# Optimization experiments

Measured on AMD Instinct MI355X. Metric: run time of the kernel, lower is better.

Reference implementation:

```python
import jax, jax.numpy as jnp
import numpy as np

N = 50000   # nodes
E = 800000  # edges (avg degree 16)
F_IN, F_HID, F_OUT = 4, 64, 1


def setup_inputs() -> dict:
    key = jax.random.key(0)
    k1, k2, k3, k4 = jax.random.split(key, 4)
    x = jax.random.normal(k1, (N, F_IN), dtype=jnp.float32)
    edge_index = jax.random.randint(k2, (2, E), 0, N, dtype=jnp.int64)
    W1 = jax.random.normal(k3, (F_IN, F_HID), dtype=jnp.float32) * (1.0 / np.sqrt(F_IN))
    b1 = jnp.zeros((F_HID,), dtype=jnp.float32)
    W2 = jax.random.normal(k4, (F_HID, F_OUT), dtype=jnp.float32) * (1.0 / np.sqrt(F_HID))
    b2 = jnp.zeros((F_OUT,), dtype=jnp.float32)
    return {"x": x, "edge_index": edge_index, "W1": W1, "b1": b1, "W2": W2, "b2": b2}


def _gcn_conv(h, W, b, src, dst, norm, n_nodes):
    # h: [N, F_in] -> linear -> gather src -> scale by norm -> scatter-add at dst
    m = (h @ W)[src] * norm[:, None]          # [E+N, F_out]
    out = jax.ops.segment_sum(m, dst, num_segments=n_nodes)
    return out + b


def reference(x, edge_index, W1, b1, W2, b2):
    n = x.shape[0]
    loops = jnp.arange(n, dtype=edge_index.dtype)
    src = jnp.concatenate([edge_index[0], loops])  # add self loops (PyG default)
    dst = jnp.concatenate([edge_index[1], loops])
    # symmetric normalization: deg computed at target (col) as in PyG gcn_norm
    deg = jax.ops.segment_sum(jnp.ones_like(dst, dtype=x.dtype), dst, num_segments=n)
    dis = jnp.where(deg > 0, deg ** -0.5, 0.0)
    norm = dis[src] * dis[dst]                      # [E+N]

    h = jax.nn.relu(_gcn_conv(x, W1, b1, src, dst, norm, n))
    # F.dropout with training=False (inference) is identity
    out = _gcn_conv(h, W2, b2, src, dst, norm, n)
    return jax.nn.sigmoid(out)                      # [N, 1]
```

## Files before the change

kernel.cpp:

```cpp
#include <hip/hip_runtime.h>


#define FH 64
#define NPC 256
#define NBC_MAX 256
#define CHB 8192
#define EPT 32
#define BCAP 8192
#define NPF 64

__global__ void k_fill(const int* __restrict__ src, const int* __restrict__ dst,
                       int* __restrict__ bcnt, unsigned int* __restrict__ ebuf,
                       int E, int nbc) {
    __shared__ int h[NBC_MAX];
    __shared__ int resv[NBC_MAX];
    int t = threadIdx.x;
    if (t < nbc) h[t] = 0;
    __syncthreads();
    int base = blockIdx.x * CHB;
    unsigned int pe[EPT];
    #pragma unroll
    for (int k = 0; k < EPT; ++k) {
        int e = base + k * 256 + t;
        if (e < E) {
            int d = dst[e];
            pe[k] = ((unsigned)d << 16) | (unsigned)src[e];
            atomicAdd(&h[d >> 8], 1);
        } else {
            pe[k] = 0xffffffffu;
        }
    }
    __syncthreads();
    if (t < nbc) {
        int c = h[t];
        resv[t] = c ? atomicAdd(&bcnt[t], c) : 0;
        h[t] = 0;
    }
    __syncthreads();
    #pragma unroll
    for (int k = 0; k < EPT; ++k) {
        if (pe[k] != 0xffffffffu) {
            int b = pe[k] >> 24;
            int idx = resv[b] + atomicAdd(&h[b], 1);
            if (idx < BCAP) ebuf[(size_t)b * BCAP + idx] = pe[k];
        }
    }
}

__global__ void k_finish1(const unsigned int* __restrict__ ebuf,
                          const int* __restrict__ bcnt,
                          const float* __restrict__ x, float* __restrict__ dis,
                          float* __restrict__ xd, int N) {
    __shared__ int lc[NPF];
    int f = blockIdx.x, t = threadIdx.x;
    int cb = f >> 2, w = f & 3;
    if (t < NPF) lc[t] = 0;
    __syncthreads();
    int c = min(bcnt[cb], BCAP);
    const unsigned int* eb = ebuf + (size_t)cb * BCAP;
    for (int j = t; j < c; j += 256) {
        int local = (eb[j] >> 16) & 255;
        if ((local >> 6) == w) atomicAdd(&lc[local & 63], 1);
    }
    __syncthreads();
    int node = f * NPF + t;
    if (t < NPF && node < N) {
        float dn = rsqrtf((float)(lc[t] + 1));
        dis[node] = dn;
        float4 xv = *reinterpret_cast<const float4*>(x + (size_t)node * 4);
        float4 o;
        o.x = dn * xv.x; o.y = dn * xv.y; o.z = dn * xv.z; o.w = dn * xv.w;
        *reinterpret_cast<float4*>(xd + (size_t)node * 4) = o;
    }
}

__global__ void k_agg(const unsigned int* __restrict__ ebuf,
                      const int* __restrict__ bcnt,
                      const float* __restrict__ xd, const float* __restrict__ dis,
                      const float* __restrict__ W1, const float* __restrict__ b1,
                      const float* __restrict__ W2, float* __restrict__ q, int N) {
    __shared__ float y4[NPF * 5];
    __shared__ float sW[4 * FH];
    __shared__ float sb1[FH];
    __shared__ float sW2[FH];
    int f = blockIdx.x, t = threadIdx.x;
    int cb = f >> 2, w = f & 3;
    sW[t] = W1[t];
    if (t < FH) { sb1[t] = b1[t]; sW2[t] = W2[t]; }
    if (t < NPF * 5) y4[t] = 0.0f;
    if (t + 256 < NPF * 5) y4[t + 256] = 0.0f;
    __syncthreads();
    int c = min(bcnt[cb], BCAP);
    const unsigned int* eb = ebuf + (size_t)cb * BCAP;
    for (int j = t; j < c; j += 256) {
        unsigned int pe = eb[j];
        int local = (pe >> 16) & 255;
        if ((local >> 6) == w) {
            int s = pe & 0xffff;
            float4 xv = *reinterpret_cast<const float4*>(xd + (size_t)s * 4);
            int l = local & 63;
            atomicAdd(&y4[l * 5 + 0], xv.x);
            atomicAdd(&y4[l * 5 + 1], xv.y);
            atomicAdd(&y4[l * 5 + 2], xv.z);
            atomicAdd(&y4[l * 5 + 3], xv.w);
        }
    }
    __syncthreads();
    int node = f * NPF + t;
    if (t < NPF && node < N) {
        float dn = dis[node];
        float4 xv = *reinterpret_cast<const float4*>(xd + (size_t)node * 4);
        float u0 = dn * (y4[t * 5 + 0] + xv.x);
        float u1 = dn * (y4[t * 5 + 1] + xv.y);
        float u2 = dn * (y4[t * 5 + 2] + xv.z);
        float u3 = dn * (y4[t * 5 + 3] + xv.w);
        float acc = 0.0f;
        #pragma unroll 8
        for (int ff = 0; ff < FH; ++ff) {
            float hh = u0 * sW[ff] + u1 * sW[FH + ff] + u2 * sW[2 * FH + ff] + u3 * sW[3 * FH + ff] + sb1[ff];
            hh = fmaxf(hh, 0.0f);
            acc += hh * sW2[ff];
        }
        q[node] = acc * dn;
    }
}

__global__ void k_layer2(const unsigned int* __restrict__ ebuf,
                         const int* __restrict__ bcnt,
                         const float* __restrict__ q, const float* __restrict__ dis,
                         const float* __restrict__ b2, float* __restrict__ out, int N) {
    __shared__ float qt[NPF];
    __shared__ float sb2;
    int f = blockIdx.x, t = threadIdx.x;
    int cb = f >> 2, w = f & 3;
    if (t == 0) sb2 = b2[0];
    if (t < NPF) qt[t] = 0.0f;
    __syncthreads();
    int c = min(bcnt[cb], BCAP);
    const unsigned int* eb = ebuf + (size_t)cb * BCAP;
    for (int j = t; j < c; j += 256) {
        unsigned int pe = eb[j];
        int local = (pe >> 16) & 255;
        if ((local >> 6) == w)
            atomicAdd(&qt[local & 63], q[pe & 0xffff]);
    }
    __syncthreads();
    int node = f * NPF + t;
    if (t < NPF && node < N) {
        float v = dis[node] * (q[node] + qt[t]) + sb2;
        out[node] = 1.0f / (1.0f + __expf(-v));
    }
}

extern "C" void kernel_launch(void* const* d_in, const int* in_sizes, int n_in,
                              void* d_out, int out_size, void* d_ws, size_t ws_size,
                              hipStream_t stream) {
    const float* x   = (const float*)d_in[0];
    const int*   ei  = (const int*)d_in[1];
    const float* W1  = (const float*)d_in[2];
    const float* b1  = (const float*)d_in[3];
    const float* W2  = (const float*)d_in[4];
    const float* b2  = (const float*)d_in[5];
    float* out = (float*)d_out;

    int N = in_sizes[0] / 4;
    int E = in_sizes[1] / 2;
    const int* src = ei;
    const int* dst = ei + E;
    int nbc = (N + NPC - 1) / NPC;
    int nbe = (E + CHB - 1) / CHB;
    int nbf = nbc * 4;

    char* ws = (char*)d_ws;
    size_t off = 0;
    auto alloc = [&](size_t bytes) {
        void* p = ws + off;
        off = (off + bytes + 255) & ~(size_t)255;
        return p;
    };
    float*        dis  = (float*)alloc((size_t)N * 4);
    float*        xd   = (float*)alloc((size_t)N * 16);
    float*        q    = (float*)alloc((size_t)N * 4);
    int*          bcnt = (int*)alloc((size_t)NBC_MAX * 4);
    unsigned int* ebuf = (unsigned int*)alloc((size_t)nbc * BCAP * 4);
    (void)ws_size;

    hipMemsetAsync(bcnt, 0, (size_t)NBC_MAX * 4, stream);

    k_fill<<<nbe, 256, 0, stream>>>(src, dst, bcnt, ebuf, E, nbc);
    k_finish1<<<nbf, 256, 0, stream>>>(ebuf, bcnt, x, dis, xd, N);
    k_agg<<<nbf, 256, 0, stream>>>(ebuf, bcnt, xd, dis, W1, b1, W2, q, N);
    k_layer2<<<nbf, 256, 0, stream>>>(ebuf, bcnt, q, dis, b2, out, N);
}
```

Measured before the change: 129.9 us.

## Process each dst bucket with one 1024-thread block instead of four filtered blocks

Each bucket of 256 destination nodes is now handled by a single 1024-thread block, replacing four 256-thread blocks that each rescanned the whole bucket and kept only a quarter of the edges. This removes the 4x redundant reads of the edge buffer and the per-edge filter branch. The MLP epilogue in k_agg is split across 4 threads per node, with the partial sums combined by shuffles. The cost is far fewer blocks (about 196) on a GPU with many CUs, plus more LDS atomic contention per block.

```diff
diff --git a/kernel.cpp b/kernel.cpp
--- a/kernel.cpp
+++ b/kernel.cpp
@@ -7,7 +7,6 @@
 #define CHB 8192
 #define EPT 32
 #define BCAP 8192
-#define NPF 64
 
 __global__ void k_fill(const int* __restrict__ src, const int* __restrict__ dst,
                        int* __restrict__ bcnt, unsigned int* __restrict__ ebuf,
@@ -47,24 +46,21 @@
     }
 }
 
-__global__ void k_finish1(const unsigned int* __restrict__ ebuf,
-                          const int* __restrict__ bcnt,
-                          const float* __restrict__ x, float* __restrict__ dis,
-                          float* __restrict__ xd, int N) {
-    __shared__ int lc[NPF];
-    int f = blockIdx.x, t = threadIdx.x;
-    int cb = f >> 2, w = f & 3;
-    if (t < NPF) lc[t] = 0;
+__global__ void __launch_bounds__(1024) k_finish1(
+        const unsigned int* __restrict__ ebuf, const int* __restrict__ bcnt,
+        const float* __restrict__ x, float* __restrict__ dis,
+        float* __restrict__ xd, int N) {
+    __shared__ int lc[NPC];
+    int cb = blockIdx.x, t = threadIdx.x;
+    if (t < NPC) lc[t] = 0;
     __syncthreads();
     int c = min(bcnt[cb], BCAP);
     const unsigned int* eb = ebuf + (size_t)cb * BCAP;
-    for (int j = t; j < c; j += 256) {
-        int local = (eb[j] >> 16) & 255;
-        if ((local >> 6) == w) atomicAdd(&lc[local & 63], 1);
-    }
+    for (int j = t; j < c; j += 1024)
+        atomicAdd(&lc[(eb[j] >> 16) & (NPC - 1)], 1);
     __syncthreads();
-    int node = f * NPF + t;
-    if (t < NPF && node < N) {
+    int node = cb * NPC + t;
+    if (t < NPC && node < N) {
         float dn = rsqrtf((float)(lc[t] + 1));
         dis[node] = dn;
         float4 xv = *reinterpret_cast<const float4*>(x + (size_t)node * 4);
@@ -74,79 +70,75 @@
     }
 }
 
-__global__ void k_agg(const unsigned int* __restrict__ ebuf,
-                      const int* __restrict__ bcnt,
-                      const float* __restrict__ xd, const float* __restrict__ dis,
-                      const float* __restrict__ W1, const float* __restrict__ b1,
-                      const float* __restrict__ W2, float* __restrict__ q, int N) {
-    __shared__ float y4[NPF * 5];
+__global__ void __launch_bounds__(1024) k_agg(
+        const unsigned int* __restrict__ ebuf, const int* __restrict__ bcnt,
+        const float* __restrict__ xd, const float* __restrict__ dis,
+        const float* __restrict__ W1, const float* __restrict__ b1,
+        const float* __restrict__ W2, float* __restrict__ q, int N) {
+    __shared__ float y4[NPC * 5];
     __shared__ float sW[4 * FH];
     __shared__ float sb1[FH];
     __shared__ float sW2[FH];
-    int f = blockIdx.x, t = threadIdx.x;
-    int cb = f >> 2, w = f & 3;
-    sW[t] = W1[t];
-    if (t < FH) { sb1[t] = b1[t]; sW2[t] = W2[t]; }
-    if (t < NPF * 5) y4[t] = 0.0f;
-    if (t + 256 < NPF * 5) y4[t + 256] = 0.0f;
+    int cb = blockIdx.x, t = threadIdx.x;
+    if (t < 4 * FH) sW[t] = W1[t];
+    else if (t < 5 * FH) sb1[t - 4 * FH] = b1[t - 4 * FH];
+    else if (t < 6 * FH) sW2[t - 5 * FH] = W2[t - 5 * FH];
+    if (t < NPC * 5 - 1024) y4[t + 1024] = 0.0f;
+    y4[t] = 0.0f;
     __syncthreads();
     int c = min(bcnt[cb], BCAP);
     const unsigned int* eb = ebuf + (size_t)cb * BCAP;
-    for (int j = t; j < c; j += 256) {
+    for (int j = t; j < c; j += 1024) {
         unsigned int pe = eb[j];
-        int local = (pe >> 16) & 255;
-        if ((local >> 6) == w) {
-            int s = pe & 0xffff;
-            float4 xv = *reinterpret_cast<const float4*>(xd + (size_t)s * 4);
-            int l = local & 63;
-            atomicAdd(&y4[l * 5 + 0], xv.x);
-            atomicAdd(&y4[l * 5 + 1], xv.y);
-            atomicAdd(&y4[l * 5 + 2], xv.z);
-            atomicAdd(&y4[l * 5 + 3], xv.w);
-        }
+        int s = pe & 0xffff;
+        int l = (pe >> 16) & (NPC - 1);
+        float4 xv = *reinterpret_cast<const float4*>(xd + (size_t)s * 4);
+        atomicAdd(&y4[l * 5 + 0], xv.x);
+        atomicAdd(&y4[l * 5 + 1], xv.y);
+        atomicAdd(&y4[l * 5 + 2], xv.z);
+        atomicAdd(&y4[l * 5 + 3], xv.w);
     }
     __syncthreads();
-    int node = f * NPF + t;
-    if (t < NPF && node < N) {
+    int l = t >> 2, r = t & 3;
+    int node = cb * NPC + l;
+    if (node < N) {
         float dn = dis[node];
         float4 xv = *reinterpret_cast<const float4*>(xd + (size_t)node * 4);
-        float u0 = dn * (y4[t * 5 + 0] + xv.x);
-        float u1 = dn * (y4[t * 5 + 1] + xv.y);
-        float u2 = dn * (y4[t * 5 + 2] + xv.z);
-        float u3 = dn * (y4[t * 5 + 3] + xv.w);
+        float u0 = dn * (y4[l * 5 + 0] + xv.x);
+        float u1 = dn * (y4[l * 5 + 1] + xv.y);
+        float u2 = dn * (y4[l * 5 + 2] + xv.z);
+        float u3 = dn * (y4[l * 5 + 3] + xv.w);
         float acc = 0.0f;
-        #pragma unroll 8
-        for (int ff = 0; ff < FH; ++ff) {
-            float hh = u0 * sW[ff] + u1 * sW[FH + ff] + u2 * sW[2 * FH + ff] + u3 * sW[3 * FH + ff] + sb1[ff];
+        int f0 = r * 16;
+        #pragma unroll
+        for (int f = f0; f < f0 + 16; ++f) {
+            float hh = u0 * sW[f] + u1 * sW[FH + f] + u2 * sW[2 * FH + f] + u3 * sW[3 * FH + f] + sb1[f];
             hh = fmaxf(hh, 0.0f);
-            acc += hh * sW2[ff];
+            acc += hh * sW2[f];
         }
-        q[node] = acc * dn;
+        acc += __shfl_xor(acc, 1, 64);
+        acc += __shfl_xor(acc, 2, 64);
+        if (r == 0) q[node] = acc * dn;
     }
 }
 
-__global__ void k_layer2(const unsigned int* __restrict__ ebuf,
-                         const int* __restrict__ bcnt,
-                         const float* __restrict__ q, const float* __restrict__ dis,
-                         const float* __restrict__ b2, float* __restrict__ out, int N) {
-    __shared__ float qt[NPF];
+__global__ void __launch_bounds__(1024) k_layer2(
+        const unsigned int* __restrict__ ebuf, const int* __restrict__ bcnt,
+        const float* __restrict__ q, const float* __restrict__ dis,
+        const float* __restrict__ b2, float* __restrict__ out, int N) {
+    __shared__ float qt[NPC];
     __shared__ float sb2;
-    int f = blockIdx.x, t = threadIdx.x;
-    int cb = f >> 2, w = f & 3;
+    int cb = blockIdx.x, t = threadIdx.x;
     if (t == 0) sb2 = b2[0];
-    if (t < NPF) qt[t] = 0.0f;
+    if (t < NPC) qt[t] = 0.0f;
     __syncthreads();
     int c = min(bcnt[cb], BCAP);
     const unsigned int* eb = ebuf + (size_t)cb * BCAP;
-    for (int j = t; j < c; j += 256) {
-        unsigned int pe = eb[j];
-        int local = (pe >> 16) & 255;
-        if ((local >> 6) == w)
-            atomicAdd(&qt[local & 63], q[pe & 0xffff]);
-    }
+    for (int j = t; j < c; j += 1024)
+        atomicAdd(&qt[(eb[j] >> 16) & (NPC - 1)], q[eb[j] & 0xffff]);
     __syncthreads();
-    int node = f * NPF + t;
-    if (t < NPF && node < N) {
+    int node = cb * NPC + t;
+    if (t < NPC && node < N) {
         float v = dis[node] * (q[node] + qt[t]) + sb2;
         out[node] = 1.0f / (1.0f + __expf(-v));
     }
@@ -169,7 +161,6 @@
     const int* dst = ei + E;
     int nbc = (N + NPC - 1) / NPC;
     int nbe = (E + CHB - 1) / CHB;
-    int nbf = nbc * 4;
 
     char* ws = (char*)d_ws;
     size_t off = 0;
@@ -188,7 +179,7 @@
     hipMemsetAsync(bcnt, 0, (size_t)NBC_MAX * 4, stream);
 
     k_fill<<<nbe, 256, 0, stream>>>(src, dst, bcnt, ebuf, E, nbc);
-    k_finish1<<<nbf, 256, 0, stream>>>(ebuf, bcnt, x, dis, xd, N);
-    k_agg<<<nbf, 256, 0, stream>>>(ebuf, bcnt, xd, dis, W1, b1, W2, q, N);
-    k_layer2<<<nbf, 256, 0, stream>>>(ebuf, bcnt, q, dis, b2, out, N);
+    k_finish1<<<nbc, 1024, 0, stream>>>(ebuf, bcnt, x, dis, xd, N);
+    k_agg<<<nbc, 1024, 0, stream>>>(ebuf, bcnt, xd, dis, W1, b1, W2, q, N);
+    k_layer2<<<nbc, 1024, 0, stream>>>(ebuf, bcnt, q, dis, b2, out, N);
 }
```

New measurement: 122.3 us. 1.06x faster.
